# Kernel optimization log

Hardware: AMD Instinct MI355X
Metric: run time of the kernel (lower is better)

## Reference

```python
import jax, jax.numpy as jnp
import numpy as np

ALPHA = -10.0  # softmax sharpness on |x - bin| distances
TAU = 0.0
TAU2 = 0.0
EPS = 1e-10

B, F, L, K = 32, 64, 1024, 32


def setup_inputs() -> dict:
    key = jax.random.key(0)
    k1, k2 = jax.random.split(key)
    x = jax.random.normal(k1, (B, F, L), dtype=jnp.float32)
    bins = jax.random.normal(k2, (K,), dtype=jnp.float32)
    return {"x": x, "bins": bins}


def reference(x, bins):
    # dist: [B, F, L, K] = |x[..., None] - bins|
    dist = jnp.abs(x[..., None] - bins)
    # soft assignment over the K bins (training path of the module)
    soft = jax.nn.softmax(ALPHA * dist, axis=-1)
    assignment = soft + EPS

    # weighted quantization loss: sum of per-bin mean of sqrt(assignment)
    quant = jnp.sum(jnp.mean(jnp.sqrt(assignment), axis=(0, 1, 2)))
    weighted_quant_loss = jnp.stack([quant, jnp.float32(TAU2)])[None, :]  # [1, 2]

    # code entropy of average assignment distribution
    p = jnp.mean(assignment, axis=(0, 1, 2))  # [K]
    code_entropy = -jnp.sum(p * jnp.log(p))
    weighted_code_entropy = jnp.stack([code_entropy, jnp.float32(TAU)])[None, :]  # [1, 2]

    # soft reconstruction against the bins: [B, F, L]
    bit_code = jnp.einsum('bflk,k->bfl', assignment, bins)
    return bit_code, weighted_code_entropy, weighted_quant_loss
```

## Files before the change

kernel.cpp:

```cpp
#include <hip/hip_runtime.h>

#define K      32
#define TPB    256
#define NB     2048
#define EPT    4
#define NTOT   (32 * 64 * 1024)
#define STRIDE (TPB * NB)

__device__ __forceinline__ float wave_reduce_sum(float v) {
#pragma unroll
  for (int m = 1; m < 64; m <<= 1) v += __shfl_xor(v, m, 64);
  return v;
}

__device__ __forceinline__ float to_sgpr(float v) {
  return __int_as_float(__builtin_amdgcn_readfirstlane(__float_as_int(v)));
}

__global__ __launch_bounds__(TPB)
void ssq_main(const float* __restrict__ x, const float* __restrict__ bins,
              float* __restrict__ out, float* __restrict__ partials) {
  const int tid  = threadIdx.x;
  const int base = blockIdx.x * TPB + tid;

  float binv[K];
#pragma unroll
  for (int k = 0; k < K; ++k) binv[k] = to_sgpr(bins[k]);
  float binsum = 0.f;
#pragma unroll
  for (int k = 0; k < K; ++k) binsum += binv[k];
  const float epsb = 1e-10f * binsum;

  float xs[EPT];
#pragma unroll
  for (int e = 0; e < EPT; ++e) xs[e] = x[base + e * STRIDE];

  float sAcc[K];
#pragma unroll
  for (int k = 0; k < K; ++k) sAcc[k] = 0.f;
  float q = 0.f;

  const float Ch = -7.213475204444817f;

#pragma unroll 1
  for (int e = 0; e < EPT; ++e) {
    const float xv = xs[e];
    float t[K];
    float s0 = 0.f, s1 = 0.f, h0 = 0.f, h1 = 0.f, b0 = 0.f, b1 = 0.f;
#pragma unroll
    for (int k = 0; k < K; k += 2) {
      float ha = __builtin_amdgcn_exp2f(Ch * fabsf(xv - binv[k + 0]));
      float hb = __builtin_amdgcn_exp2f(Ch * fabsf(xv - binv[k + 1]));
      float ta = ha * ha, tb = hb * hb;
      t[k + 0] = ta; t[k + 1] = tb;
      s0 += ta; s1 += tb;
      h0 += ha; h1 += hb;
      b0 = fmaf(ta, binv[k + 0], b0);
      b1 = fmaf(tb, binv[k + 1], b1);
    }
    const float s    = s0 + s1;
    const float inv  = __builtin_amdgcn_rcpf(s);
    q = fmaf(h0 + h1, __builtin_amdgcn_rsqf(s), q);
    out[base + e * STRIDE] = fmaf(b0 + b1, inv, epsb);
#pragma unroll
    for (int k = 0; k < K; ++k) sAcc[k] = fmaf(t[k], inv, sAcc[k]);
  }

  __shared__ float red[4][K + 1];
  const int lane = tid & 63, wv = tid >> 6;
#pragma unroll
  for (int k = 0; k < K; ++k) {
    float v = wave_reduce_sum(sAcc[k]);
    if (lane == 0) red[wv][k] = v;
  }
  {
    float v = wave_reduce_sum(q);
    if (lane == 0) red[wv][K] = v;
  }
  __syncthreads();
  if (tid < K + 1) {
    float v = red[0][tid] + red[1][tid] + red[2][tid] + red[3][tid];
    partials[tid * NB + blockIdx.x] = v;
  }
}

__global__ __launch_bounds__(TPB)
void ssq_reduce(const float* __restrict__ partials, float* __restrict__ sums) {
  const float* p = partials + blockIdx.x * NB;
  const int tid  = threadIdx.x;
  float s = 0.f;
#pragma unroll
  for (int j = 0; j < NB / TPB; ++j) s += p[tid + j * TPB];
  s = wave_reduce_sum(s);
  __shared__ float red[4];
  if ((tid & 63) == 0) red[tid >> 6] = s;
  __syncthreads();
  if (tid == 0) sums[blockIdx.x] = red[0] + red[1] + red[2] + red[3];
}

__global__ void ssq_final(const float* __restrict__ sums, float* __restrict__ out) {
  const int lane = threadIdx.x;
  float e = 0.f;
  if (lane < K) {
    float p = sums[lane] * (1.0f / (float)NTOT) + 1e-10f;
    e = -p * __logf(p);
  }
  e = wave_reduce_sum(e);
  if (lane == 0) {
    out[NTOT + 0] = e;
    out[NTOT + 1] = 0.f;
    out[NTOT + 2] = sums[K] * (1.0f / (float)NTOT);
    out[NTOT + 3] = 0.f;
  }
}

extern "C" void kernel_launch(void* const* d_in, const int* in_sizes, int n_in,
                              void* d_out, int out_size, void* d_ws, size_t ws_size,
                              hipStream_t stream) {
  const float* x    = (const float*)d_in[0];
  const float* bins = (const float*)d_in[1];
  float* out        = (float*)d_out;
  float* partials   = (float*)d_ws;
  float* sums       = partials + (K + 1) * NB;

  ssq_main  <<<NB,    TPB, 0, stream>>>(x, bins, out, partials);
  ssq_reduce<<<K + 1, TPB, 0, stream>>>(partials, sums);
  ssq_final <<<1,     64,  0, stream>>>(sums, out);
}
```

Baseline: 87.24 us.

## Split bins across thread pairs and double elements per thread

Each element is now handled by a pair of adjacent lanes, each computing 16 of the 32 bins and combining the sum, weighted sum and per-bin accumulators with lane shuffles. EPT doubles so the total work per thread stays balanced, and the end-of-block reduction now shuffles only 16 accumulators across lanes. Bins are loaded per lane into VGPRs rather than broadcast as scalars. This cuts the per-thread accumulator register footprint and the number of cross-lane reduction steps, at the cost of extra shuffles per element and only half the lanes doing the output store.

```diff
diff --git a/kernel.cpp b/kernel.cpp
--- a/kernel.cpp
+++ b/kernel.cpp
@@ -1,11 +1,12 @@
 #include <hip/hip_runtime.h>
 
 #define K      32
+#define KH     16
 #define TPB    256
 #define NB     2048
-#define EPT    4
+#define EPT    8
 #define NTOT   (32 * 64 * 1024)
-#define STRIDE (TPB * NB)
+#define PSTRIDE (NB * (TPB / 2))
 
 __device__ __forceinline__ float wave_reduce_sum(float v) {
 #pragma unroll
@@ -13,31 +14,35 @@
   return v;
 }
 
-__device__ __forceinline__ float to_sgpr(float v) {
-  return __int_as_float(__builtin_amdgcn_readfirstlane(__float_as_int(v)));
+__device__ __forceinline__ float pair_lane_reduce(float v) {
+#pragma unroll
+  for (int m = 2; m < 64; m <<= 1) v += __shfl_xor(v, m, 64);
+  return v;
 }
 
 __global__ __launch_bounds__(TPB)
 void ssq_main(const float* __restrict__ x, const float* __restrict__ bins,
               float* __restrict__ out, float* __restrict__ partials) {
   const int tid  = threadIdx.x;
-  const int base = blockIdx.x * TPB + tid;
+  const int half = tid & 1;
+  const int pslot = blockIdx.x * (TPB / 2) + (tid >> 1);
 
-  float binv[K];
+  float binv[KH];
 #pragma unroll
-  for (int k = 0; k < K; ++k) binv[k] = to_sgpr(bins[k]);
-  float binsum = 0.f;
+  for (int j = 0; j < KH; ++j) binv[j] = bins[KH * half + j];
+  float bs_local = 0.f;
 #pragma unroll
-  for (int k = 0; k < K; ++k) binsum += binv[k];
+  for (int j = 0; j < KH; ++j) bs_local += binv[j];
+  const float binsum = bs_local + __shfl_xor(bs_local, 1, 64);
   const float epsb = 1e-10f * binsum;
 
   float xs[EPT];
 #pragma unroll
-  for (int e = 0; e < EPT; ++e) xs[e] = x[base + e * STRIDE];
+  for (int e = 0; e < EPT; ++e) xs[e] = x[pslot + e * PSTRIDE];
 
-  float sAcc[K];
+  float sAcc[KH];
 #pragma unroll
-  for (int k = 0; k < K; ++k) sAcc[k] = 0.f;
+  for (int j = 0; j < KH; ++j) sAcc[j] = 0.f;
   float q = 0.f;
 
   const float Ch = -7.213475204444817f;
@@ -45,33 +50,36 @@
 #pragma unroll 1
   for (int e = 0; e < EPT; ++e) {
     const float xv = xs[e];
-    float t[K];
+    float t[KH];
     float s0 = 0.f, s1 = 0.f, h0 = 0.f, h1 = 0.f, b0 = 0.f, b1 = 0.f;
 #pragma unroll
-    for (int k = 0; k < K; k += 2) {
-      float ha = __builtin_amdgcn_exp2f(Ch * fabsf(xv - binv[k + 0]));
-      float hb = __builtin_amdgcn_exp2f(Ch * fabsf(xv - binv[k + 1]));
+    for (int j = 0; j < KH; j += 2) {
+      float ha = __builtin_amdgcn_exp2f(Ch * fabsf(xv - binv[j + 0]));
+      float hb = __builtin_amdgcn_exp2f(Ch * fabsf(xv - binv[j + 1]));
       float ta = ha * ha, tb = hb * hb;
-      t[k + 0] = ta; t[k + 1] = tb;
+      t[j + 0] = ta; t[j + 1] = tb;
       s0 += ta; s1 += tb;
       h0 += ha; h1 += hb;
-      b0 = fmaf(ta, binv[k + 0], b0);
-      b1 = fmaf(tb, binv[k + 1], b1);
+      b0 = fmaf(ta, binv[j + 0], b0);
+      b1 = fmaf(tb, binv[j + 1], b1);
     }
-    const float s    = s0 + s1;
-    const float inv  = __builtin_amdgcn_rcpf(s);
-    q = fmaf(h0 + h1, __builtin_amdgcn_rsqf(s), q);
-    out[base + e * STRIDE] = fmaf(b0 + b1, inv, epsb);
+    const float s_loc = s0 + s1;
+    const float b_loc = b0 + b1;
+    const float s_full = s_loc + __shfl_xor(s_loc, 1, 64);
+    const float b_full = b_loc + __shfl_xor(b_loc, 1, 64);
+    const float inv = __builtin_amdgcn_rcpf(s_full);
+    q = fmaf(h0 + h1, __builtin_amdgcn_rsqf(s_full), q);
+    if (half == 0) out[pslot + e * PSTRIDE] = fmaf(b_full, inv, epsb);
 #pragma unroll
-    for (int k = 0; k < K; ++k) sAcc[k] = fmaf(t[k], inv, sAcc[k]);
+    for (int j = 0; j < KH; ++j) sAcc[j] = fmaf(t[j], inv, sAcc[j]);
   }
 
   __shared__ float red[4][K + 1];
   const int lane = tid & 63, wv = tid >> 6;
 #pragma unroll
-  for (int k = 0; k < K; ++k) {
-    float v = wave_reduce_sum(sAcc[k]);
-    if (lane == 0) red[wv][k] = v;
+  for (int j = 0; j < KH; ++j) {
+    float v = pair_lane_reduce(sAcc[j]);
+    if (lane < 2) red[wv][KH * lane + j] = v;
   }
   {
     float v = wave_reduce_sum(q);
```

New measurement: 84.10 us. 1.04x faster.
